# Performance work log

Hardware: AMD Instinct MI355X
Metric: run time of the kernel (lower is better)

## Reference

```python
import jax, jax.numpy as jnp
import numpy as np

B, S, D, H = 2, 2048, 1024, 16
DK = D // H


def setup_inputs() -> dict:
    key = jax.random.key(0)
    ks = jax.random.split(key, 12)
    scale = 1.0 / np.sqrt(D)
    inp = {
        "q": jax.random.normal(ks[0], (B, S, D), dtype=jnp.float32),
        "k": jax.random.normal(ks[1], (B, S, D), dtype=jnp.float32),
        "v": jax.random.normal(ks[2], (B, S, D), dtype=jnp.float32),
        "mask": jax.random.randint(ks[3], (B, 1, 1, S), 0, 2, dtype=jnp.int32),
        "Wq": jax.random.normal(ks[4], (D, D), dtype=jnp.float32) * scale,
        "bq": jnp.zeros((D,), dtype=jnp.float32),
        "Wk": jax.random.normal(ks[5], (D, D), dtype=jnp.float32) * scale,
        "bk": jnp.zeros((D,), dtype=jnp.float32),
        "Wv": jax.random.normal(ks[6], (D, D), dtype=jnp.float32) * scale,
        "bv": jnp.zeros((D,), dtype=jnp.float32),
        "Wo": jax.random.normal(ks[7], (D, D), dtype=jnp.float32) * scale,
        "bo": jnp.zeros((D,), dtype=jnp.float32),
    }
    return inp


def reference(q, k, v, mask, Wq, bq, Wk, bk, Wv, bv, Wo, bo):
    # Linear projections (torch nn.Linear: x @ W.T + b)
    query = q @ Wq.T + bq                      # [B,S,D]
    key = k @ Wk.T + bk
    value = v @ Wv.T + bv
    # split heads -> [B,H,S,DK]
    def split(x):
        return x.reshape(B, S, H, DK).transpose(0, 2, 1, 3)
    qh, kh, vh = split(query), split(key), split(value)
    # scaled dot-product attention with additive mask
    scores = jnp.einsum("bhqd,bhkd->bhqk", qh, kh) / jnp.sqrt(jnp.float32(DK))
    scores = jnp.where(mask == 0, jnp.float32(-1e9), scores)
    attn = jax.nn.softmax(scores, axis=-1)     # [B,H,S,S]
    out = jnp.einsum("bhqk,bhkd->bhqd", attn, vh)
    out = out.transpose(0, 2, 1, 3).reshape(B, S, D)
    return out @ Wo.T + bo
```

## Files before the change

### kernel.cpp

```cpp
#include <hip/hip_runtime.h>


constexpr int BB = 2;
constexpr int SS = 2048;
constexpr int DD = 1024;
constexpr int HH = 16;
constexpr int DKK = 64;

typedef float f32x4 __attribute__((ext_vector_type(4)));
typedef __bf16 bf16x8 __attribute__((ext_vector_type(8)));
typedef short s16x8 __attribute__((ext_vector_type(8)));
typedef short s16x4 __attribute__((ext_vector_type(4)));

#define DEV static __device__ __forceinline__

DEV f32x4 mfma16(s16x8 a, s16x8 b, f32x4 c) {
  return __builtin_amdgcn_mfma_f32_16x16x32_bf16(
      __builtin_bit_cast(bf16x8, a), __builtin_bit_cast(bf16x8, b), c, 0, 0, 0);
}

DEV void split1(float x, short& h, short& l) {
  unsigned u = __float_as_uint(x);
  h = (short)(u >> 16);
  float hf = __uint_as_float(u & 0xffff0000u);
  l = (short)(__float_as_uint(x - hf) >> 16);
}
DEV short f2bf_rne(float x) {
  unsigned u = __float_as_uint(x);
  return (short)((u + 0x7fffu + ((u >> 16) & 1u)) >> 16);
}
DEV s16x8 load8s(const short* p) { return *(const s16x8*)p; }

DEV void gld_lds16(const short* g, short* l) {
  __builtin_amdgcn_global_load_lds(
      (const __attribute__((address_space(1))) void*)g,
      (__attribute__((address_space(3))) void*)l, 16, 0, 0);
}

__global__ __launch_bounds__(256) void split_pair(const float* __restrict__ X,
                                                  short* __restrict__ H,
                                                  short* __restrict__ L) {
  int i = (blockIdx.x * 256 + threadIdx.x) * 4;
  float4 x = *(const float4*)(X + i);
  float xs[4] = {x.x, x.y, x.z, x.w};
  s16x4 h4, l4;
#pragma unroll
  for (int e = 0; e < 4; ++e) {
    short h, l;
    split1(xs[e], h, l);
    h4[e] = h;
    l4[e] = l;
  }
  *(s16x4*)(H + i) = h4;
  *(s16x4*)(L + i) = l4;
}

__global__ __launch_bounds__(256) void cast_rne(const float* __restrict__ X,
                                                short* __restrict__ Y) {
  int i = (blockIdx.x * 256 + threadIdx.x) * 4;
  float4 x = *(const float4*)(X + i);
  float xs[4] = {x.x, x.y, x.z, x.w};
  s16x4 y4;
#pragma unroll
  for (int e = 0; e < 4; ++e) y4[e] = f2bf_rne(xs[e]);
  *(s16x4*)(Y + i) = y4;
}

__global__ __launch_bounds__(256) void gemm_qk(
    const short* __restrict__ qAh, const short* __restrict__ qAl,
    const short* __restrict__ Wqh, const short* __restrict__ Wql,
    const float* __restrict__ bq, short* __restrict__ Qo,
    const short* __restrict__ kAh, const short* __restrict__ kAl,
    const short* __restrict__ Wkh, const short* __restrict__ Wkl,
    const float* __restrict__ bk, short* __restrict__ Kho,
    short* __restrict__ Klo) {
  __shared__ short lds[2][12288];

  const int tid = threadIdx.x;
  const int lane = tid & 63, wv = tid >> 6;
  const int lo16 = lane & 15, quad = lane >> 4;
  const int sel = blockIdx.x >> 9;
  const int bid = blockIdx.x & 511;
  const int m0 = (bid & 31) * 128;
  const int n0 = (bid >> 5) * 64;

  const short* Agh = sel ? kAh : qAh;
  const short* Agl = sel ? kAl : qAl;
  const short* Wgh = sel ? Wkh : Wqh;
  const short* Wgl = sel ? Wkl : Wql;
  const float* bias = sel ? bk : bq;

  f32x4 acc[2][4];
#pragma unroll
  for (int mt = 0; mt < 2; ++mt)
#pragma unroll
    for (int nt = 0; nt < 4; ++nt) acc[mt][nt] = f32x4{0.f, 0.f, 0.f, 0.f};

  const int rw = tid >> 2, qw = tid & 3;
  const int ra0 = tid >> 2, ra1 = (tid + 256) >> 2;

  auto stage = [&](int k0, int buf) {
    short* sAh = lds[buf];
    short* sAl = lds[buf] + 4096;
    short* sWh = lds[buf] + 8192;
    short* sWl = lds[buf] + 10240;
    gld_lds16(Wgh + (size_t)(n0 + rw) * DD + k0 + qw * 8, sWh + tid * 8);
    gld_lds16(Wgl + (size_t)(n0 + rw) * DD + k0 + qw * 8, sWl + tid * 8);
    gld_lds16(Agh + (size_t)(m0 + ra0) * DD + k0 + qw * 8, sAh + tid * 8);
    gld_lds16(Agh + (size_t)(m0 + ra1) * DD + k0 + qw * 8, sAh + (tid + 256) * 8);
    gld_lds16(Agl + (size_t)(m0 + ra0) * DD + k0 + qw * 8, sAl + tid * 8);
    gld_lds16(Agl + (size_t)(m0 + ra1) * DD + k0 + qw * 8, sAl + (tid + 256) * 8);
  };

  stage(0, 0);

  for (int kk = 0; kk < DD / 32; ++kk) {
    __syncthreads();
    if (kk + 1 < DD / 32) stage((kk + 1) * 32, (kk + 1) & 1);

    const short* sAh = lds[kk & 1];
    const short* sAl = lds[kk & 1] + 4096;
    const short* sWh = lds[kk & 1] + 8192;
    const short* sWl = lds[kk & 1] + 10240;

    s16x8 ah[2], al[2], wh[4], wl[4];
#pragma unroll
    for (int mt = 0; mt < 2; ++mt) {
      const int r = wv * 32 + mt * 16 + lo16;
      ah[mt] = *(const s16x8*)&sAh[r * 32 + quad * 8];
      al[mt] = *(const s16x8*)&sAl[r * 32 + quad * 8];
    }
#pragma unroll
    for (int nt = 0; nt < 4; ++nt) {
      const int r = nt * 16 + lo16;
      wh[nt] = *(const s16x8*)&sWh[r * 32 + quad * 8];
      wl[nt] = *(const s16x8*)&sWl[r * 32 + quad * 8];
    }
#pragma unroll
    for (int mt = 0; mt < 2; ++mt)
#pragma unroll
      for (int nt = 0; nt < 4; ++nt) {
        acc[mt][nt] = mfma16(ah[mt], wh[nt], acc[mt][nt]);
        acc[mt][nt] = mfma16(ah[mt], wl[nt], acc[mt][nt]);
        acc[mt][nt] = mfma16(al[mt], wh[nt], acc[mt][nt]);
      }
  }

#pragma unroll
  for (int mt = 0; mt < 2; ++mt)
#pragma unroll
    for (int nt = 0; nt < 4; ++nt) {
      const int n = n0 + nt * 16 + lo16;
      const float bv = bias[n];
#pragma unroll
      for (int r = 0; r < 4; ++r) {
        const int m = m0 + wv * 32 + mt * 16 + quad * 4 + r;
        const float val = acc[mt][nt][r] + bv;
        const int b = m >> 11, s = m & 2047;
        const int h = n >> 6, dk = n & 63;
        size_t idx = ((size_t)(b * HH + h) * SS + s) * DKK + dk;
        if (sel == 0) {
          Qo[idx] = f2bf_rne(val);
        } else {
          short hh, ll;
          split1(val, hh, ll);
          Kho[idx] = hh;
          Klo[idx] = ll;
        }
      }
    }
}

template <int SPLIT, int EPI>
__global__ __launch_bounds__(256) void gemm_tile(
    const short* __restrict__ Agh, const short* __restrict__ Agl,
    const short* __restrict__ Wgh, const short* __restrict__ Wgl,
    const float* __restrict__ bias, void* __restrict__ O1, void* __restrict__ O2) {
  __shared__ short lds[2][12288];

  const int tid = threadIdx.x;
  const int lane = tid & 63, wv = tid >> 6;
  const int lo16 = lane & 15, quad = lane >> 4;
  const int m0 = (blockIdx.x & 31) * 128;
  const int n0 = (blockIdx.x >> 5) * 64;

  f32x4 acc[2][4];
#pragma unroll
  for (int mt = 0; mt < 2; ++mt)
#pragma unroll
    for (int nt = 0; nt < 4; ++nt) acc[mt][nt] = f32x4{0.f, 0.f, 0.f, 0.f};

  const int rw = tid >> 2, qw = tid & 3;
  const int ra0 = tid >> 2, ra1 = (tid + 256) >> 2;

  auto stage = [&](int k0, int buf) {
    short* sAh = lds[buf];
    short* sAl = lds[buf] + 4096;
    short* sWh = lds[buf] + 8192;
    short* sWl = lds[buf] + 10240;
    gld_lds16(Wgh + (size_t)(n0 + rw) * DD + k0 + qw * 8, sWh + tid * 8);
    if constexpr (SPLIT)
      gld_lds16(Wgl + (size_t)(n0 + rw) * DD + k0 + qw * 8, sWl + tid * 8);
    gld_lds16(Agh + (size_t)(m0 + ra0) * DD + k0 + qw * 8, sAh + tid * 8);
    gld_lds16(Agh + (size_t)(m0 + ra1) * DD + k0 + qw * 8, sAh + (tid + 256) * 8);
    if constexpr (SPLIT) {
      gld_lds16(Agl + (size_t)(m0 + ra0) * DD + k0 + qw * 8, sAl + tid * 8);
      gld_lds16(Agl + (size_t)(m0 + ra1) * DD + k0 + qw * 8, sAl + (tid + 256) * 8);
    }
  };

  stage(0, 0);

  for (int kk = 0; kk < DD / 32; ++kk) {
    __syncthreads();
    if (kk + 1 < DD / 32) stage((kk + 1) * 32, (kk + 1) & 1);

    const short* sAh = lds[kk & 1];
    const short* sAl = lds[kk & 1] + 4096;
    const short* sWh = lds[kk & 1] + 8192;
    const short* sWl = lds[kk & 1] + 10240;

    s16x8 ah[2], al[2], wh[4], wl[4];
#pragma unroll
    for (int mt = 0; mt < 2; ++mt) {
      const int r = wv * 32 + mt * 16 + lo16;
      ah[mt] = *(const s16x8*)&sAh[r * 32 + quad * 8];
      if constexpr (SPLIT) al[mt] = *(const s16x8*)&sAl[r * 32 + quad * 8];
    }
#pragma unroll
    for (int nt = 0; nt < 4; ++nt) {
      const int r = nt * 16 + lo16;
      wh[nt] = *(const s16x8*)&sWh[r * 32 + quad * 8];
      if constexpr (SPLIT) wl[nt] = *(const s16x8*)&sWl[r * 32 + quad * 8];
    }
#pragma unroll
    for (int mt = 0; mt < 2; ++mt)
#pragma unroll
      for (int nt = 0; nt < 4; ++nt) {
        acc[mt][nt] = mfma16(ah[mt], wh[nt], acc[mt][nt]);
        if constexpr (SPLIT) {
          acc[mt][nt] = mfma16(ah[mt], wl[nt], acc[mt][nt]);
          acc[mt][nt] = mfma16(al[mt], wh[nt], acc[mt][nt]);
        }
      }
  }

#pragma unroll
  for (int mt = 0; mt < 2; ++mt)
#pragma unroll
    for (int nt = 0; nt < 4; ++nt) {
      const int n = n0 + nt * 16 + lo16;
      const float bv = bias[n];
#pragma unroll
      for (int r = 0; r < 4; ++r) {
        const int m = m0 + wv * 32 + mt * 16 + quad * 4 + r;
        const float val = acc[mt][nt][r] + bv;
        const int b = m >> 11, s = m & 2047;
        const int h = n >> 6, dk = n & 63;
        if constexpr (EPI == 1) {
          size_t idx = ((size_t)(b * HH + h) * DKK + dk) * SS + s;
          ((short*)O1)[idx] = f2bf_rne(val);
        } else {
          ((float*)O1)[(size_t)m * DD + n] = val;
        }
      }
    }
}

constexpr int PAD = 68;
constexpr int NKB = SS / 64;

__global__ __launch_bounds__(256, 2) void mha_attn(
    const short* __restrict__ Qh, const short* __restrict__ Kh,
    const short* __restrict__ Kl, const short* __restrict__ Vt,
    const int* __restrict__ mask, short* __restrict__ Ah,
    short* __restrict__ Al) {
  __shared__ short sKh[64 * PAD];
  __shared__ short sKl[64 * PAD];
  __shared__ short sV[64 * PAD];
  __shared__ short sP[4][32 * PAD];

  const int tid = threadIdx.x;
  const int lane = tid & 63, wv = tid >> 6;
  const int lo16 = lane & 15, quad = lane >> 4;
  const int bid = blockIdx.x;
  const int head = (bid & 7) * 4 + ((bid >> 3) & 3);
  const int qblk = bid >> 5;
  const int q0 = qblk * 128 + wv * 32;
  const int b = head >> 4;

  const size_t hbase = (size_t)head * SS;

  s16x8 qh[2][2];
#pragma unroll
  for (int rt = 0; rt < 2; ++rt) {
    size_t qb = (hbase + q0 + rt * 16 + lo16) * DKK + quad * 8;
#pragma unroll
    for (int c = 0; c < 2; ++c) qh[rt][c] = load8s(Qh + qb + c * 32);
  }

  f32x4 Oacc[2][4];
#pragma unroll
  for (int rt = 0; rt < 2; ++rt)
#pragma unroll
    for (int t = 0; t < 4; ++t) Oacc[rt][t] = f32x4{0.f, 0.f, 0.f, 0.f};
  float lsum[2][4];
#pragma unroll
  for (int rt = 0; rt < 2; ++rt)
#pragma unroll
    for (int r = 0; r < 4; ++r) lsum[rt][r] = 0.f;

  const int srow = tid >> 2;
  const int scol0 = (tid & 3) * 8;

  s16x8 rKh[2], rKl[2], rV[2];
#pragma unroll
  for (int i = 0; i < 2; ++i) {
    const int sc_ = scol0 + i * 32;
    rKh[i] = load8s(Kh + (hbase + srow) * DKK + sc_);
    rKl[i] = load8s(Kl + (hbase + srow) * DKK + sc_);
    rV[i] = load8s(Vt + ((size_t)head * DKK + srow) * SS + sc_);
  }

  for (int kb = 0; kb < NKB; ++kb) {
    const int k0g = kb * 64;
#pragma unroll
    for (int i = 0; i < 2; ++i) {
      const int sc_ = scol0 + i * 32;
      *(s16x8*)&sKh[srow * PAD + sc_] = rKh[i];
      *(s16x8*)&sKl[srow * PAD + sc_] = rKl[i];
      *(s16x8*)&sV[srow * PAD + sc_] = rV[i];
    }
    __syncthreads();

    if (kb + 1 < NKB) {
      const int k0n = k0g + 64;
#pragma unroll
      for (int i = 0; i < 2; ++i) {
        const int sc_ = scol0 + i * 32;
        rKh[i] = load8s(Kh + (hbase + k0n + srow) * DKK + sc_);
        rKl[i] = load8s(Kl + (hbase + k0n + srow) * DKK + sc_);
        rV[i] = load8s(Vt + ((size_t)head * DKK + srow) * SS + k0n + sc_);
      }
    }

    f32x4 sc4[2][4];
    int mv[4];
#pragma unroll
    for (int sub = 0; sub < 4; ++sub) {
      mv[sub] = mask[b * SS + k0g + sub * 16 + lo16];
      sc4[0][sub] = f32x4{0.f, 0.f, 0.f, 0.f};
      sc4[1][sub] = f32x4{0.f, 0.f, 0.f, 0.f};
      const int krow = sub * 16 + lo16;
#pragma unroll
      for (int c = 0; c < 2; ++c) {
        s16x8 kh = *(const s16x8*)&sKh[krow * PAD + c * 32 + quad * 8];
        s16x8 kl = *(const s16x8*)&sKl[krow * PAD + c * 32 + quad * 8];
#pragma unroll
        for (int rt = 0; rt < 2; ++rt) {
          sc4[rt][sub] = mfma16(qh[rt][c], kh, sc4[rt][sub]);
          sc4[rt][sub] = mfma16(qh[rt][c], kl, sc4[rt][sub]);
        }
      }
    }

#pragma unroll
    for (int rt = 0; rt < 2; ++rt)
#pragma unroll
      for (int sub = 0; sub < 4; ++sub)
#pragma unroll
        for (int r = 0; r < 4; ++r) {
          float p = __expf(sc4[rt][sub][r] * 0.125f);
          p = mv[sub] ? p : 0.f;
          lsum[rt][r] += p;
          sP[wv][(rt * 16 + quad * 4 + r) * PAD + sub * 16 + lo16] = f2bf_rne(p);
        }

    s16x8 pa[2][2];
#pragma unroll
    for (int rt = 0; rt < 2; ++rt)
#pragma unroll
      for (int c = 0; c < 2; ++c)
        pa[rt][c] = *(const s16x8*)&sP[wv][(rt * 16 + lo16) * PAD + c * 32 + quad * 8];
#pragma unroll
    for (int t = 0; t < 4; ++t)
#pragma unroll
      for (int c = 0; c < 2; ++c) {
        s16x8 vb = *(const s16x8*)&sV[(t * 16 + lo16) * PAD + c * 32 + quad * 8];
#pragma unroll
        for (int rt = 0; rt < 2; ++rt)
          Oacc[rt][t] = mfma16(pa[rt][c], vb, Oacc[rt][t]);
      }
    __syncthreads();
  }

  const int h = head & 15;
#pragma unroll
  for (int rt = 0; rt < 2; ++rt)
#pragma unroll
    for (int r = 0; r < 4; ++r) {
      float s = lsum[rt][r];
#pragma unroll
      for (int off = 1; off < 16; off <<= 1) s += __shfl_xor(s, off);
      const float rinv = 1.0f / s;
#pragma unroll
      for (int t = 0; t < 4; ++t) {
        const float val = Oacc[rt][t][r] * rinv;
        const int row = q0 + rt * 16 + quad * 4 + r;
        const int col = h * DKK + t * 16 + lo16;
        const size_t idx = ((size_t)b * SS + row) * DD + col;
        short hh, ll;
        split1(val, hh, ll);
        Ah[idx] = hh;
        Al[idx] = ll;
      }
    }
}

extern "C" void kernel_launch(void* const* d_in, const int* in_sizes, int n_in,
                              void* d_out, int out_size, void* d_ws, size_t ws_size,
                              hipStream_t stream) {
  const float* q = (const float*)d_in[0];
  const float* k = (const float*)d_in[1];
  const float* v = (const float*)d_in[2];
  const int* mask = (const int*)d_in[3];
  const float* Wq = (const float*)d_in[4];
  const float* bq = (const float*)d_in[5];
  const float* Wk = (const float*)d_in[6];
  const float* bk = (const float*)d_in[7];
  const float* Wv = (const float*)d_in[8];
  const float* bv = (const float*)d_in[9];
  const float* Wo = (const float*)d_in[10];
  const float* bo = (const float*)d_in[11];

  char* ws = (char*)d_ws;
  size_t off = 0;
  auto take = [&](size_t bytes) {
    char* p = ws + off;
    off += (bytes + 255) & ~(size_t)255;
    return p;
  };
  const size_t WE = (size_t)DD * DD;
  const size_t TE = (size_t)BB * SS * DD;

  short* Wqh = (short*)take(WE * 2);
  short* Wql = (short*)take(WE * 2);
  short* Wkh = (short*)take(WE * 2);
  short* Wkl = (short*)take(WE * 2);
  short* Wvh = (short*)take(WE * 2);
  short* Woh = (short*)take(WE * 2);
  short* Wol = (short*)take(WE * 2);
  short* qH = (short*)take(TE * 2);
  short* qL = (short*)take(TE * 2);
  short* kH = (short*)take(TE * 2);
  short* kL = (short*)take(TE * 2);
  short* Qh = (short*)take(TE * 2);
  short* Kh = (short*)take(TE * 2);
  short* Kl = (short*)take(TE * 2);
  (void)ws_size;
  short* vH = qH;
  short* Vt = qL;
  short* aH = kH;
  short* aL = kL;

  split_pair<<<1024, 256, 0, stream>>>(Wq, Wqh, Wql);
  split_pair<<<1024, 256, 0, stream>>>(Wk, Wkh, Wkl);
  split_pair<<<1024, 256, 0, stream>>>(Wo, Woh, Wol);
  cast_rne<<<1024, 256, 0, stream>>>(Wv, Wvh);

  split_pair<<<4096, 256, 0, stream>>>(q, qH, qL);
  split_pair<<<4096, 256, 0, stream>>>(k, kH, kL);

  gemm_qk<<<1024, 256, 0, stream>>>(qH, qL, Wqh, Wql, bq, Qh,
                                    kH, kL, Wkh, Wkl, bk, Kh, Kl);

  cast_rne<<<4096, 256, 0, stream>>>(v, vH);
  gemm_tile<0, 1><<<512, 256, 0, stream>>>(vH, nullptr, Wvh, nullptr, bv, Vt, nullptr);

  mha_attn<<<512, 256, 0, stream>>>(Qh, Kh, Kl, Vt, mask, aH, aL);

  gemm_tile<1, 2><<<512, 256, 0, stream>>>(aH, aL, Woh, Wol, bo, d_out, nullptr);
}
```

Baseline: 336.3 us.

## Halve attention query tile per wave to double grid size and occupancy

Each wave in the attention kernel now handles 16 query rows instead of 32, so a block covers 64 queries and the grid doubles to 1024 blocks with a launch bound of 4 blocks per CU. The P staging buffer shrinks accordingly, and register use drops. The exponential now uses exp2f with the log2(e) factor folded into the scale. The aim is more waves for latency hiding; the cost is that each K/V tile loaded into shared memory is reused by half as many queries, doubling K/V load traffic.

```diff
diff --git a/kernel.cpp b/kernel.cpp
--- a/kernel.cpp
+++ b/kernel.cpp
@@ -269,8 +269,9 @@
 
 constexpr int PAD = 68;
 constexpr int NKB = SS / 64;
-
-__global__ __launch_bounds__(256, 2) void mha_attn(
+constexpr float EXPSC = 0.125f * 1.4426950408889634f;
+
+__global__ __launch_bounds__(256, 4) void mha_attn(
     const short* __restrict__ Qh, const short* __restrict__ Kh,
     const short* __restrict__ Kl, const short* __restrict__ Vt,
     const int* __restrict__ mask, short* __restrict__ Ah,
@@ -278,7 +279,7 @@
   __shared__ short sKh[64 * PAD];
   __shared__ short sKl[64 * PAD];
   __shared__ short sV[64 * PAD];
-  __shared__ short sP[4][32 * PAD];
+  __shared__ short sP[4][16 * PAD];
 
   const int tid = threadIdx.x;
   const int lane = tid & 63, wv = tid >> 6;
@@ -286,29 +287,22 @@
   const int bid = blockIdx.x;
   const int head = (bid & 7) * 4 + ((bid >> 3) & 3);
   const int qblk = bid >> 5;
-  const int q0 = qblk * 128 + wv * 32;
+  const int q0 = qblk * 64 + wv * 16;
   const int b = head >> 4;
 
   const size_t hbase = (size_t)head * SS;
 
-  s16x8 qh[2][2];
-#pragma unroll
-  for (int rt = 0; rt < 2; ++rt) {
-    size_t qb = (hbase + q0 + rt * 16 + lo16) * DKK + quad * 8;
-#pragma unroll
-    for (int c = 0; c < 2; ++c) qh[rt][c] = load8s(Qh + qb + c * 32);
-  }
-
-  f32x4 Oacc[2][4];
-#pragma unroll
-  for (int rt = 0; rt < 2; ++rt)
-#pragma unroll
-    for (int t = 0; t < 4; ++t) Oacc[rt][t] = f32x4{0.f, 0.f, 0.f, 0.f};
-  float lsum[2][4];
-#pragma unroll
-  for (int rt = 0; rt < 2; ++rt)
-#pragma unroll
-    for (int r = 0; r < 4; ++r) lsum[rt][r] = 0.f;
+  s16x8 qh[2];
+  {
+    size_t qb = (hbase + q0 + lo16) * DKK + quad * 8;
+    qh[0] = load8s(Qh + qb);
+    qh[1] = load8s(Qh + qb + 32);
+  }
+
+  f32x4 Oacc[4];
+#pragma unroll
+  for (int t = 0; t < 4; ++t) Oacc[t] = f32x4{0.f, 0.f, 0.f, 0.f};
+  float lsum[4] = {0.f, 0.f, 0.f, 0.f};
 
   const int srow = tid >> 2;
   const int scol0 = (tid & 3) * 8;
@@ -344,77 +338,65 @@
       }
     }
 
-    f32x4 sc4[2][4];
+    f32x4 sc4[4];
     int mv[4];
 #pragma unroll
     for (int sub = 0; sub < 4; ++sub) {
       mv[sub] = mask[b * SS + k0g + sub * 16 + lo16];
-      sc4[0][sub] = f32x4{0.f, 0.f, 0.f, 0.f};
-      sc4[1][sub] = f32x4{0.f, 0.f, 0.f, 0.f};
+      sc4[sub] = f32x4{0.f, 0.f, 0.f, 0.f};
       const int krow = sub * 16 + lo16;
 #pragma unroll
       for (int c = 0; c < 2; ++c) {
         s16x8 kh = *(const s16x8*)&sKh[krow * PAD + c * 32 + quad * 8];
         s16x8 kl = *(const s16x8*)&sKl[krow * PAD + c * 32 + quad * 8];
-#pragma unroll
-        for (int rt = 0; rt < 2; ++rt) {
-          sc4[rt][sub] = mfma16(qh[rt][c], kh, sc4[rt][sub]);
-          sc4[rt][sub] = mfma16(qh[rt][c], kl, sc4[rt][sub]);
-        }
-      }
-    }
-
-#pragma unroll
-    for (int rt = 0; rt < 2; ++rt)
-#pragma unroll
-      for (int sub = 0; sub < 4; ++sub)
-#pragma unroll
-        for (int r = 0; r < 4; ++r) {
-          float p = __expf(sc4[rt][sub][r] * 0.125f);
-          p = mv[sub] ? p : 0.f;
-          lsum[rt][r] += p;
-          sP[wv][(rt * 16 + quad * 4 + r) * PAD + sub * 16 + lo16] = f2bf_rne(p);
-        }
-
-    s16x8 pa[2][2];
-#pragma unroll
-    for (int rt = 0; rt < 2; ++rt)
-#pragma unroll
-      for (int c = 0; c < 2; ++c)
-        pa[rt][c] = *(const s16x8*)&sP[wv][(rt * 16 + lo16) * PAD + c * 32 + quad * 8];
+        sc4[sub] = mfma16(qh[c], kh, sc4[sub]);
+        sc4[sub] = mfma16(qh[c], kl, sc4[sub]);
+      }
+    }
+
+#pragma unroll
+    for (int sub = 0; sub < 4; ++sub)
+#pragma unroll
+      for (int r = 0; r < 4; ++r) {
+        float p = exp2f(sc4[sub][r] * EXPSC);
+        p = mv[sub] ? p : 0.f;
+        lsum[r] += p;
+        sP[wv][(quad * 4 + r) * PAD + sub * 16 + lo16] = f2bf_rne(p);
+      }
+
+    s16x8 pa[2];
+#pragma unroll
+    for (int c = 0; c < 2; ++c)
+      pa[c] = *(const s16x8*)&sP[wv][lo16 * PAD + c * 32 + quad * 8];
 #pragma unroll
     for (int t = 0; t < 4; ++t)
 #pragma unroll
       for (int c = 0; c < 2; ++c) {
         s16x8 vb = *(const s16x8*)&sV[(t * 16 + lo16) * PAD + c * 32 + quad * 8];
-#pragma unroll
-        for (int rt = 0; rt < 2; ++rt)
-          Oacc[rt][t] = mfma16(pa[rt][c], vb, Oacc[rt][t]);
+        Oacc[t] = mfma16(pa[c], vb, Oacc[t]);
       }
     __syncthreads();
   }
 
   const int h = head & 15;
 #pragma unroll
-  for (int rt = 0; rt < 2; ++rt)
-#pragma unroll
-    for (int r = 0; r < 4; ++r) {
-      float s = lsum[rt][r];
-#pragma unroll
-      for (int off = 1; off < 16; off <<= 1) s += __shfl_xor(s, off);
-      const float rinv = 1.0f / s;
-#pragma unroll
-      for (int t = 0; t < 4; ++t) {
-        const float val = Oacc[rt][t][r] * rinv;
-        const int row = q0 + rt * 16 + quad * 4 + r;
-        const int col = h * DKK + t * 16 + lo16;
-        const size_t idx = ((size_t)b * SS + row) * DD + col;
-        short hh, ll;
-        split1(val, hh, ll);
-        Ah[idx] = hh;
-        Al[idx] = ll;
-      }
-    }
+  for (int r = 0; r < 4; ++r) {
+    float s = lsum[r];
+#pragma unroll
+    for (int off = 1; off < 16; off <<= 1) s += __shfl_xor(s, off);
+    const float rinv = 1.0f / s;
+#pragma unroll
+    for (int t = 0; t < 4; ++t) {
+      const float val = Oacc[t][r] * rinv;
+      const int row = q0 + quad * 4 + r;
+      const int col = h * DKK + t * 16 + lo16;
+      const size_t idx = ((size_t)b * SS + row) * DD + col;
+      short hh, ll;
+      split1(val, hh, ll);
+      Ah[idx] = hh;
+      Al[idx] = ll;
+    }
+  }
 }
 
 extern "C" void kernel_launch(void* const* d_in, const int* in_sizes, int n_in,
@@ -477,7 +459,7 @@
   cast_rne<<<4096, 256, 0, stream>>>(v, vH);
   gemm_tile<0, 1><<<512, 256, 0, stream>>>(vH, nullptr, Wvh, nullptr, bv, Vt, nullptr);
 
-  mha_attn<<<512, 256, 0, stream>>>(Qh, Kh, Kl, Vt, mask, aH, aL);
+  mha_attn<<<1024, 256, 0, stream>>>(Qh, Kh, Kl, Vt, mask, aH, aL);
 
   gemm_tile<1, 2><<<512, 256, 0, stream>>>(aH, aL, Woh, Wol, bo, d_out, nullptr);
 }
```

After: 350.7 us. 4.3% more time.

## Load K/V fragments directly from global memory in attention, drop LDS staging

Applied to the files above, without the earlier changes.

The attention kernel no longer stages K-high, K-low and V tiles through shared memory with register prefetch and block-wide barriers. Each wave now loads its MFMA operand fragments straight from global memory (the L2 cache), which removes both __syncthreads per key block and the LDS traffic. The exponential is also rewritten as exp2f with a folded log2(e) scale. The cost is that each of the 4 waves in a block re-reads the same K/V data, which raises global/L2 load traffic and exposes latency because there is no explicit prefetch.

```diff
diff --git a/kernel.cpp b/kernel.cpp
--- a/kernel.cpp
+++ b/kernel.cpp
@@ -269,15 +269,13 @@
 
 constexpr int PAD = 68;
 constexpr int NKB = SS / 64;
+constexpr float EXPSC = 0.125f * 1.4426950408889634f;
 
 __global__ __launch_bounds__(256, 2) void mha_attn(
     const short* __restrict__ Qh, const short* __restrict__ Kh,
     const short* __restrict__ Kl, const short* __restrict__ Vt,
     const int* __restrict__ mask, short* __restrict__ Ah,
     short* __restrict__ Al) {
-  __shared__ short sKh[64 * PAD];
-  __shared__ short sKl[64 * PAD];
-  __shared__ short sV[64 * PAD];
   __shared__ short sP[4][32 * PAD];
 
   const int tid = threadIdx.x;
@@ -310,39 +308,8 @@
 #pragma unroll
     for (int r = 0; r < 4; ++r) lsum[rt][r] = 0.f;
 
-  const int srow = tid >> 2;
-  const int scol0 = (tid & 3) * 8;
-
-  s16x8 rKh[2], rKl[2], rV[2];
-#pragma unroll
-  for (int i = 0; i < 2; ++i) {
-    const int sc_ = scol0 + i * 32;
-    rKh[i] = load8s(Kh + (hbase + srow) * DKK + sc_);
-    rKl[i] = load8s(Kl + (hbase + srow) * DKK + sc_);
-    rV[i] = load8s(Vt + ((size_t)head * DKK + srow) * SS + sc_);
-  }
-
   for (int kb = 0; kb < NKB; ++kb) {
     const int k0g = kb * 64;
-#pragma unroll
-    for (int i = 0; i < 2; ++i) {
-      const int sc_ = scol0 + i * 32;
-      *(s16x8*)&sKh[srow * PAD + sc_] = rKh[i];
-      *(s16x8*)&sKl[srow * PAD + sc_] = rKl[i];
-      *(s16x8*)&sV[srow * PAD + sc_] = rV[i];
-    }
-    __syncthreads();
-
-    if (kb + 1 < NKB) {
-      const int k0n = k0g + 64;
-#pragma unroll
-      for (int i = 0; i < 2; ++i) {
-        const int sc_ = scol0 + i * 32;
-        rKh[i] = load8s(Kh + (hbase + k0n + srow) * DKK + sc_);
-        rKl[i] = load8s(Kl + (hbase + k0n + srow) * DKK + sc_);
-        rV[i] = load8s(Vt + ((size_t)head * DKK + srow) * SS + k0n + sc_);
-      }
-    }
 
     f32x4 sc4[2][4];
     int mv[4];
@@ -351,11 +318,11 @@
       mv[sub] = mask[b * SS + k0g + sub * 16 + lo16];
       sc4[0][sub] = f32x4{0.f, 0.f, 0.f, 0.f};
       sc4[1][sub] = f32x4{0.f, 0.f, 0.f, 0.f};
-      const int krow = sub * 16 + lo16;
+      const size_t krow = hbase + k0g + sub * 16 + lo16;
 #pragma unroll
       for (int c = 0; c < 2; ++c) {
-        s16x8 kh = *(const s16x8*)&sKh[krow * PAD + c * 32 + quad * 8];
-        s16x8 kl = *(const s16x8*)&sKl[krow * PAD + c * 32 + quad * 8];
+        s16x8 kh = load8s(Kh + krow * DKK + c * 32 + quad * 8);
+        s16x8 kl = load8s(Kl + krow * DKK + c * 32 + quad * 8);
 #pragma unroll
         for (int rt = 0; rt < 2; ++rt) {
           sc4[rt][sub] = mfma16(qh[rt][c], kh, sc4[rt][sub]);
@@ -364,13 +331,21 @@
       }
     }
 
+    s16x8 vbr[4][2];
+#pragma unroll
+    for (int t = 0; t < 4; ++t)
+#pragma unroll
+      for (int c = 0; c < 2; ++c)
+        vbr[t][c] = load8s(Vt + ((size_t)head * DKK + t * 16 + lo16) * SS +
+                           k0g + c * 32 + quad * 8);
+
 #pragma unroll
     for (int rt = 0; rt < 2; ++rt)
 #pragma unroll
       for (int sub = 0; sub < 4; ++sub)
 #pragma unroll
         for (int r = 0; r < 4; ++r) {
-          float p = __expf(sc4[rt][sub][r] * 0.125f);
+          float p = exp2f(sc4[rt][sub][r] * EXPSC);
           p = mv[sub] ? p : 0.f;
           lsum[rt][r] += p;
           sP[wv][(rt * 16 + quad * 4 + r) * PAD + sub * 16 + lo16] = f2bf_rne(p);
@@ -386,12 +361,10 @@
     for (int t = 0; t < 4; ++t)
 #pragma unroll
       for (int c = 0; c < 2; ++c) {
-        s16x8 vb = *(const s16x8*)&sV[(t * 16 + lo16) * PAD + c * 32 + quad * 8];
 #pragma unroll
         for (int rt = 0; rt < 2; ++rt)
-          Oacc[rt][t] = mfma16(pa[rt][c], vb, Oacc[rt][t]);
-      }
-    __syncthreads();
+          Oacc[rt][t] = mfma16(pa[rt][c], vbr[t][c], Oacc[rt][t]);
+      }
   }
 
   const int h = head & 15;
```

After: 417.8 us. 1.24x slower.
